# Optimization experiments

Measured on AMD Instinct MI355X. Metric: run time of the kernel, lower is better.

## Reference

```python
import math
import jax, jax.numpy as jnp
import numpy as np

PATCH_NUMS = (1, 2, 3, 4, 5, 6, 8, 10, 13, 16)
_lens = [p * p for p in PATCH_NUMS]
_cum = np.concatenate([[0], np.cumsum(_lens)])
BEGIN_ENDS = [(int(_cum[i]), int(_cum[i + 1])) for i in range(len(PATCH_NUMS))]
L_TOTAL = int(_cum[-1])  # 680

B, C = 32, 1024
S, P, M, R, NCAT = 10, 8, 4, 8, 22
SLOTS = P * M  # 32 slots per scale
MEM_RANK = 64
ALPHA_HID = 128


def setup_inputs() -> dict:
    key = jax.random.key(0)
    ks = jax.random.split(key, 24)
    inp = {}
    inp['x'] = jax.random.normal(ks[0], (B, L_TOTAL, C), jnp.float32)
    # -1 means CFG-unconditional sample (no category memory)
    inp['category_ids'] = jax.random.randint(ks[1], (B,), -1, NCAT)
    # shared memory, orthogonal-ish init rescaled to xavier std sqrt(2/(C+C))
    inp['shared_memory'] = jax.random.normal(ks[2], (S, SLOTS, C)) * math.sqrt(1.0 / C)
    inp['cat_A'] = jax.random.normal(ks[3], (NCAT, S, R)) * 0.01
    inp['cat_B'] = jax.random.normal(ks[4], (S, R, SLOTS * C)) * (1.0 / math.sqrt(R))
    inp['cat_emb'] = jax.random.normal(ks[5], (NCAT, C)) * 0.02
    inp['scale_emb'] = jax.random.normal(ks[6], (S, C)) * 0.02
    inp['Wq'] = jax.random.normal(ks[7], (C, C)) * (1.0 / math.sqrt(C))
    inp['Wk'] = jax.random.normal(ks[8], (C, C)) * (1.0 / math.sqrt(C))
    inp['Wv'] = jax.random.normal(ks[9], (C, C)) * (1.0 / math.sqrt(C))
    inp['aW1'] = jax.random.normal(ks[10], (3 * C, ALPHA_HID)) * (1.0 / math.sqrt(3 * C))
    inp['ab1'] = jnp.zeros((ALPHA_HID,), jnp.float32)
    inp['aW2'] = jax.random.normal(ks[11], (ALPHA_HID, 1)) * 0.01  # init zeros in torch; small random to exercise math
    inp['ab2'] = jnp.full((1,), -1.0, jnp.float32)
    inp['kW1'] = jax.random.normal(ks[12], (C, MEM_RANK)) * (1.0 / math.sqrt(C))
    inp['kb1'] = jnp.zeros((MEM_RANK,), jnp.float32)
    inp['kW2'] = jax.random.normal(ks[13], (MEM_RANK, C)) * (1.0 / math.sqrt(MEM_RANK))
    inp['kb2'] = jnp.zeros((C,), jnp.float32)
    inp['vW1'] = jax.random.normal(ks[14], (C, MEM_RANK)) * (1.0 / math.sqrt(C))
    inp['vb1'] = jnp.zeros((MEM_RANK,), jnp.float32)
    inp['vW2'] = jax.random.normal(ks[15], (MEM_RANK, C)) * (1.0 / math.sqrt(MEM_RANK))
    inp['vb2'] = jnp.zeros((C,), jnp.float32)
    inp['gk_logit'] = jnp.float32(-2.0)  # block_idx=0, depth=16
    inp['gv_logit'] = jnp.float32(-2.0)
    inp['log_temp'] = jnp.float32(math.log(0.1))
    return inp


def reference(x, category_ids, shared_memory, cat_A, cat_B, cat_emb, scale_emb,
              Wq, Wk, Wv, aW1, ab1, aW2, ab2,
              kW1, kb1, kW2, kb2, vW1, vb1, vW2, vb2,
              gk_logit, gv_logit, log_temp):
    Bb, L, Cc = x.shape
    temp = jnp.clip(jnp.exp(log_temp), 0.05, 1.0)
    inv_sqrt_c = 1.0 / math.sqrt(Cc)

    query = x @ Wq                              # [B, L, C]
    shared_k = shared_memory @ Wk               # [S, slots, C]
    shared_v = shared_memory @ Wv

    valid = (category_ids >= 0)                 # [B]
    cid = jnp.clip(category_ids, 0, None)
    a_all = cat_A[cid]                          # [B, S, R]
    ce = cat_emb[cid]                           # [B, C]

    outs = []
    for i, (s, e) in enumerate(BEGIN_ENDS):
        q = query[:, s:e, :]                    # [B, Ls, C]
        Ls = e - s
        V = i + 1                               # visible scales
        # --- shared retrieval over visible slots ---
        ks_ = shared_k[:V].reshape(V * SLOTS, Cc)
        vs_ = shared_v[:V].reshape(V * SLOTS, Cc)
        attn_s = jax.nn.softmax((q @ ks_.T) * inv_sqrt_c / temp, axis=-1)
        o_s = attn_s @ vs_                      # [B, Ls, C]
        # --- per-category memory: shared + low-rank residual ---
        delta = jnp.einsum('bvr,vrd->bvd', a_all[:, :V], cat_B[:V])
        delta = delta.reshape(Bb, V, SLOTS, Cc)
        cat_mem = (shared_memory[:V][None] + delta).reshape(Bb, V * SLOTS, Cc)
        kc = cat_mem @ Wk                       # [B, Vs, C]
        vc = cat_mem @ Wv
        attn_c = jax.nn.softmax(jnp.einsum('bld,bsd->bls', q, kc) * inv_sqrt_c / temp, axis=-1)
        o_c = jnp.einsum('bls,bsd->bld', attn_c, vc)
        # --- learned alpha blend (zeroed for invalid / CFG categories) ---
        ai = jnp.concatenate([
            q,
            jnp.broadcast_to(ce[:, None, :], (Bb, Ls, Cc)),
            jnp.broadcast_to(scale_emb[i][None, None, :], (Bb, Ls, Cc)),
        ], axis=-1)                             # [B, Ls, 3C]
        h = jax.nn.gelu(ai @ aW1 + ab1, approximate=False)
        alpha = jax.nn.sigmoid(h @ aW2 + ab2)   # [B, Ls, 1]
        alpha = jnp.where(valid[:, None, None], alpha, 0.0)
        outs.append(o_s + alpha * (o_c - o_s))

    mem = jnp.concatenate(outs, axis=1)         # [B, L, C]
    mem_k = jax.nn.sigmoid(gk_logit) * ((mem @ kW1 + kb1) @ kW2 + kb2)
    mem_v = jax.nn.sigmoid(gv_logit) * ((mem @ vW1 + vb1) @ vW2 + vb2)
    zero = jnp.float32(0.0)
    return mem_k, mem_v, zero, zero
```

## Files before the change

### kernel.cpp

```cpp
#include <hip/hip_runtime.h>
#include <math.h>

#define NB 32
#define NC 1024
#define LTOT 680

typedef unsigned short u16;
typedef __bf16 bf16x8 __attribute__((ext_vector_type(8)));
typedef float floatx4 __attribute__((ext_vector_type(4)));

__device__ __forceinline__ u16 f2bf(float f)
{
    union { float f; unsigned u; } v; v.f = f;
    unsigned u = v.u;
    u += 0x7FFFu + ((u >> 16) & 1u);
    return (u16)(u >> 16);
}

__device__ __forceinline__ float bf2f(unsigned u)
{
    union { unsigned u; float f; } v; v.u = u << 16; return v.f;
}

__device__ __forceinline__ void gload16(const u16* g, u16* l)
{
    typedef __attribute__((address_space(1))) const void gv_t;
    typedef __attribute__((address_space(3))) void lv_t;
    __builtin_amdgcn_global_load_lds(
        (gv_t*)(unsigned long long)(const void*)g,
        (lv_t*)(unsigned int)(unsigned long long)(void*)l,
        16, 0, 0);
}

__device__ __forceinline__ void slot_decode(int s, int* prow, int* pcq)
{
    *prow = ((s >> 7) << 4) | (s & 15);
    *pcq  = (((s >> 6) & 1) << 2) | ((s >> 4) & 3);
}

__device__ __forceinline__ void slot_decode256(int s, int* prow, int* pcq)
{
    *prow = ((s >> 6) << 4) | (s & 15);
    *pcq  = (s >> 4) & 3;
}

#define WAIT_VM8()  asm volatile("s_waitcnt vmcnt(8)" ::: "memory")
#define WAIT_VM4()  asm volatile("s_waitcnt vmcnt(4)" ::: "memory")
#define WAIT_VM0()  asm volatile("s_waitcnt vmcnt(0)" ::: "memory")
#define BAR()       __builtin_amdgcn_s_barrier()
#define SCHEDB()    __builtin_amdgcn_sched_barrier(0)

template<int OUTBF>
__global__ __launch_bounds__(512) void gemm256(
    const u16* __restrict__ A, const u16* __restrict__ BT,
    float* __restrict__ C, int M, int N, int K, int lda,
    const float* __restrict__ bias, const float* __restrict__ scale_logit)
{
    __shared__ __align__(16) u16 As[2][8192];
    __shared__ __align__(16) u16 Bs[2][8192];

    const int tid  = threadIdx.x;
    const int m0   = blockIdx.y << 8;
    const int n0   = blockIdx.x << 8;
    const int wave = tid >> 6;
    const int lane = tid & 63;
    const int mh   = wave & 1;
    const int nh   = wave >> 1;
    const int lbase = (wave << 6) * 8;

    const u16* aSrc[2];
    const u16* bSrc[2];
#pragma unroll
    for (int p = 0; p < 2; ++p) {
        int s = tid + (p << 9), row, cq;
        slot_decode256(s, &row, &cq);
        int gr = m0 + row; if (gr > M - 1) gr = M - 1;
        aSrc[p] = A + (size_t)gr * lda + (cq << 3);
        int gn = n0 + row; if (gn > N - 1) gn = N - 1;
        bSrc[p] = BT + (size_t)gn * K + (cq << 3);
    }

    floatx4 acc[8][4];
#pragma unroll
    for (int i = 0; i < 8; ++i)
#pragma unroll
        for (int j = 0; j < 4; ++j) acc[i][j] = (floatx4){0.f, 0.f, 0.f, 0.f};

#pragma unroll
    for (int p = 0; p < 2; ++p) gload16(aSrc[p], &As[0][lbase + (p << 12)]);
#pragma unroll
    for (int p = 0; p < 2; ++p) gload16(bSrc[p], &Bs[0][lbase + (p << 12)]);

    const int nt = K >> 5;
    for (int t = 0; t < nt; ++t) {
        const int cur = t & 1;
        if (t + 1 < nt) {
            const int kk = (t + 1) << 5;
#pragma unroll
            for (int p = 0; p < 2; ++p) gload16(aSrc[p] + kk, &As[cur ^ 1][lbase + (p << 12)]);
#pragma unroll
            for (int p = 0; p < 2; ++p) gload16(bSrc[p] + kk, &Bs[cur ^ 1][lbase + (p << 12)]);
            WAIT_VM4();
        } else {
            WAIT_VM0();
        }
        BAR(); SCHEDB();
        {
            bf16x8 a[8], b[4];
#pragma unroll
            for (int i = 0; i < 8; ++i)
                a[i] = *(const bf16x8*)&As[cur][((((mh << 3) + i) << 6) + lane) * 8];
#pragma unroll
            for (int j = 0; j < 4; ++j)
                b[j] = *(const bf16x8*)&Bs[cur][((((nh << 2) + j) << 6) + lane) * 8];
#pragma unroll
            for (int i = 0; i < 8; ++i)
#pragma unroll
                for (int j = 0; j < 4; ++j)
                    acc[i][j] = __builtin_amdgcn_mfma_f32_16x16x32_bf16(a[i], b[j], acc[i][j], 0, 0, 0);
        }
        SCHEDB(); BAR();
    }

    float scale = 1.f;
    if (scale_logit) scale = 1.f / (1.f + __expf(-scale_logit[0]));
    const int col = lane & 15, rquad = lane >> 4;
#pragma unroll
    for (int i = 0; i < 8; ++i) {
#pragma unroll
        for (int j = 0; j < 4; ++j) {
#pragma unroll
            for (int r = 0; r < 4; ++r) {
                int gr = m0 + (mh << 7) + (i << 4) + (rquad << 2) + r;
                int gc = n0 + (nh << 6) + (j << 4) + col;
                if (gr < M && gc < N) {
                    float bb = bias ? bias[gc] : 0.f;
                    float val = scale * (acc[i][j][r] + bb);
                    if (OUTBF) ((u16*)C)[(size_t)gr * N + gc] = f2bf(val);
                    else       C[(size_t)gr * N + gc] = val;
                }
            }
        }
    }
}

__global__ __launch_bounds__(512) void gemm256_logits(
    const u16* __restrict__ Q, const u16* __restrict__ skb,
    const u16* __restrict__ kcb, float* __restrict__ out)
{
    __shared__ __align__(16) u16 As[2][8192];
    __shared__ __align__(16) u16 Bs[2][8192];

    const int tid  = threadIdx.x;
    const int m0   = blockIdx.y << 8;
    const int n0   = blockIdx.x << 8;
    const int b    = blockIdx.z;
    const int wave = tid >> 6;
    const int lane = tid & 63;
    const int mh   = wave & 1;
    const int nh   = wave >> 1;
    const int lbase = (wave << 6) * 8;

    const u16* Ab = Q   + (size_t)b * 680 * 1024;
    const u16* KC = kcb + (size_t)b * 320 * 1024;

    const u16* aSrc[2];
    const u16* bSrc[2];
#pragma unroll
    for (int p = 0; p < 2; ++p) {
        int s = tid + (p << 9), row, cq;
        slot_decode256(s, &row, &cq);
        int gr = m0 + row; if (gr > 679) gr = 679;
        aSrc[p] = Ab + (size_t)gr * 1024 + (cq << 3);
        int gn = n0 + row; if (gn > 639) gn = 639;
        bSrc[p] = ((gn < 320) ? (skb + (size_t)gn * 1024)
                              : (KC + (size_t)(gn - 320) * 1024)) + (cq << 3);
    }

    floatx4 acc[8][4];
#pragma unroll
    for (int i = 0; i < 8; ++i)
#pragma unroll
        for (int j = 0; j < 4; ++j) acc[i][j] = (floatx4){0.f, 0.f, 0.f, 0.f};

#pragma unroll
    for (int p = 0; p < 2; ++p) gload16(aSrc[p], &As[0][lbase + (p << 12)]);
#pragma unroll
    for (int p = 0; p < 2; ++p) gload16(bSrc[p], &Bs[0][lbase + (p << 12)]);

    for (int t = 0; t < 32; ++t) {
        const int cur = t & 1;
        if (t < 31) {
            const int kk = (t + 1) << 5;
#pragma unroll
            for (int p = 0; p < 2; ++p) gload16(aSrc[p] + kk, &As[cur ^ 1][lbase + (p << 12)]);
#pragma unroll
            for (int p = 0; p < 2; ++p) gload16(bSrc[p] + kk, &Bs[cur ^ 1][lbase + (p << 12)]);
            WAIT_VM4();
        } else {
            WAIT_VM0();
        }
        BAR(); SCHEDB();
        {
            bf16x8 a[8], bb[4];
#pragma unroll
            for (int i = 0; i < 8; ++i)
                a[i] = *(const bf16x8*)&As[cur][((((mh << 3) + i) << 6) + lane) * 8];
#pragma unroll
            for (int j = 0; j < 4; ++j)
                bb[j] = *(const bf16x8*)&Bs[cur][((((nh << 2) + j) << 6) + lane) * 8];
#pragma unroll
            for (int i = 0; i < 8; ++i)
#pragma unroll
                for (int j = 0; j < 4; ++j)
                    acc[i][j] = __builtin_amdgcn_mfma_f32_16x16x32_bf16(a[i], bb[j], acc[i][j], 0, 0, 0);
        }
        SCHEDB(); BAR();
    }

    const int col = lane & 15, rquad = lane >> 4;
#pragma unroll
    for (int i = 0; i < 8; ++i)
#pragma unroll
        for (int j = 0; j < 4; ++j)
#pragma unroll
            for (int r = 0; r < 4; ++r) {
                int gr = m0 + (mh << 7) + (i << 4) + (rquad << 2) + r;
                int gc = n0 + (nh << 6) + (j << 4) + col;
                if (gr < 680 && gc < 640)
                    out[((size_t)b * 680 + gr) * 640 + gc] = acc[i][j][r];
            }
}

__global__ __launch_bounds__(512) void gemm256_pv(
    const u16* __restrict__ P, const u16* __restrict__ svT,
    const u16* __restrict__ vcT, u16* __restrict__ out)
{
    __shared__ __align__(16) u16 As[2][8192];
    __shared__ __align__(16) u16 Bs[2][8192];

    const int tid  = threadIdx.x;
    const int m0   = blockIdx.y << 8;
    const int n0   = blockIdx.x << 8;
    const int b    = blockIdx.z;
    const int wave = tid >> 6;
    const int lane = tid & 63;
    const int mh   = wave & 1;
    const int nh   = wave >> 1;
    const int lbase = (wave << 6) * 8;

    const u16* aSrc[2];
    const u16* bSrcS[2];
    const u16* bSrcC[2];
#pragma unroll
    for (int p = 0; p < 2; ++p) {
        int s = tid + (p << 9), row, cq;
        slot_decode256(s, &row, &cq);
        int gr = m0 + row; if (gr > 679) gr = 679;
        aSrc[p] = P + ((size_t)b * 680 + gr) * 1280 + (cq << 3);
        int gn = n0 + row;
        bSrcS[p] = svT + (size_t)gn * 320 + (cq << 3);
        bSrcC[p] = vcT + ((size_t)b * 1024 + gn) * 320 + (cq << 3);
    }

    floatx4 acc[8][4];
#pragma unroll
    for (int i = 0; i < 8; ++i)
#pragma unroll
        for (int j = 0; j < 4; ++j) acc[i][j] = (floatx4){0.f, 0.f, 0.f, 0.f};

#pragma unroll
    for (int p = 0; p < 2; ++p) gload16(aSrc[p], &As[0][lbase + (p << 12)]);
#pragma unroll
    for (int p = 0; p < 2; ++p) gload16(bSrcS[p], &Bs[0][lbase + (p << 12)]);

    for (int t = 0; t < 20; ++t) {
        const int cur = t & 1;
        if (t < 19) {
            const int tn = t + 1;
            const int kk = tn << 5;
#pragma unroll
            for (int p = 0; p < 2; ++p) gload16(aSrc[p] + kk, &As[cur ^ 1][lbase + (p << 12)]);
#pragma unroll
            for (int p = 0; p < 2; ++p) {
                const u16* bp = (tn < 10) ? (bSrcS[p] + kk) : (bSrcC[p] + ((tn - 10) << 5));
                gload16(bp, &Bs[cur ^ 1][lbase + (p << 12)]);
            }
            WAIT_VM4();
        } else {
            WAIT_VM0();
        }
        BAR(); SCHEDB();
        {
            bf16x8 a[8], bb[4];
#pragma unroll
            for (int i = 0; i < 8; ++i)
                a[i] = *(const bf16x8*)&As[cur][((((mh << 3) + i) << 6) + lane) * 8];
#pragma unroll
            for (int j = 0; j < 4; ++j)
                bb[j] = *(const bf16x8*)&Bs[cur][((((nh << 2) + j) << 6) + lane) * 8];
#pragma unroll
            for (int i = 0; i < 8; ++i)
#pragma unroll
                for (int j = 0; j < 4; ++j)
                    acc[i][j] = __builtin_amdgcn_mfma_f32_16x16x32_bf16(a[i], bb[j], acc[i][j], 0, 0, 0);
        }
        SCHEDB(); BAR();
    }

    const int col = lane & 15, rquad = lane >> 4;
#pragma unroll
    for (int i = 0; i < 8; ++i)
#pragma unroll
        for (int j = 0; j < 4; ++j)
#pragma unroll
            for (int r = 0; r < 4; ++r) {
                int gr = m0 + (mh << 7) + (i << 4) + (rquad << 2) + r;
                int gc = n0 + (nh << 6) + (j << 4) + col;
                if (gr < 680)
                    out[((size_t)b * 680 + gr) * 1024 + gc] = f2bf(acc[i][j][r]);
            }
}

template<int OUTBF>
__global__ __launch_bounds__(256) void gemm_mfma(
    const u16* __restrict__ A, const u16* __restrict__ BT,
    float* __restrict__ C, int M, int N, int K, int lda,
    const float* __restrict__ bias, const float* __restrict__ scale_logit)
{
    __shared__ __align__(16) u16 As[2][8192];
    __shared__ __align__(16) u16 Bs[2][8192];

    const int tid  = threadIdx.x;
    const int m0   = blockIdx.y << 7;
    const int n0   = blockIdx.x << 7;
    const int wave = tid >> 6;
    const int lane = tid & 63;
    const int mh   = wave & 1;
    const int nh   = wave >> 1;
    const int lbase = (wave << 6) * 8;

    const u16* aSrc[4];
    const u16* bSrc[4];
#pragma unroll
    for (int p = 0; p < 4; ++p) {
        int s = tid + (p << 8), row, cq;
        slot_decode(s, &row, &cq);
        int gr = m0 + row; if (gr > M - 1) gr = M - 1;
        aSrc[p] = A + (size_t)gr * lda + (cq << 3);
        int gn = n0 + row; if (gn > N - 1) gn = N - 1;
        bSrc[p] = BT + (size_t)gn * K + (cq << 3);
    }

    floatx4 acc[4][4];
#pragma unroll
    for (int i = 0; i < 4; ++i)
#pragma unroll
        for (int j = 0; j < 4; ++j) acc[i][j] = (floatx4){0.f, 0.f, 0.f, 0.f};

#pragma unroll
    for (int p = 0; p < 4; ++p) gload16(aSrc[p], &As[0][lbase + (p << 11)]);
#pragma unroll
    for (int p = 0; p < 4; ++p) gload16(bSrc[p], &Bs[0][lbase + (p << 11)]);

    const int nt = K >> 6;
    for (int t = 0; t < nt; ++t) {
        const int cur = t & 1;
        if (t + 1 < nt) {
            const int kk = (t + 1) << 6;
#pragma unroll
            for (int p = 0; p < 4; ++p) gload16(aSrc[p] + kk, &As[cur ^ 1][lbase + (p << 11)]);
#pragma unroll
            for (int p = 0; p < 4; ++p) gload16(bSrc[p] + kk, &Bs[cur ^ 1][lbase + (p << 11)]);
            WAIT_VM8();
        } else {
            WAIT_VM0();
        }
        BAR(); SCHEDB();
#pragma unroll
        for (int kh = 0; kh < 2; ++kh) {
            bf16x8 a[4], b[4];
#pragma unroll
            for (int i = 0; i < 4; ++i)
                a[i] = *(const bf16x8*)&As[cur][(((((mh << 2) + i) << 1) | kh) * 64 + lane) * 8];
#pragma unroll
            for (int j = 0; j < 4; ++j)
                b[j] = *(const bf16x8*)&Bs[cur][(((((nh << 2) + j) << 1) | kh) * 64 + lane) * 8];
#pragma unroll
            for (int i = 0; i < 4; ++i)
#pragma unroll
                for (int j = 0; j < 4; ++j)
                    acc[i][j] = __builtin_amdgcn_mfma_f32_16x16x32_bf16(a[i], b[j], acc[i][j], 0, 0, 0);
        }
        SCHEDB(); BAR();
    }

    float scale = 1.f;
    if (scale_logit) scale = 1.f / (1.f + __expf(-scale_logit[0]));
    const int col = lane & 15, rquad = lane >> 4;
#pragma unroll
    for (int i = 0; i < 4; ++i) {
#pragma unroll
        for (int j = 0; j < 4; ++j) {
#pragma unroll
            for (int r = 0; r < 4; ++r) {
                int gr = m0 + (mh << 6) + (i << 4) + (rquad << 2) + r;
                int gc = n0 + (nh << 6) + (j << 4) + col;
                if (gr < M && gc < N) {
                    float bb = bias ? bias[gc] : 0.f;
                    float val = scale * (acc[i][j][r] + bb);
                    if (OUTBF) ((u16*)C)[(size_t)gr * N + gc] = f2bf(val);
                    else       C[(size_t)gr * N + gc] = val;
                }
            }
        }
    }
}

__global__ __launch_bounds__(256) void gemm_halpha(
    const u16* __restrict__ Q, const u16* __restrict__ W,
    const float* __restrict__ ceW, const float* __restrict__ seW,
    const int* __restrict__ cat_ids, u16* __restrict__ h)
{
    __shared__ __align__(16) u16 As[2][8192];
    __shared__ __align__(16) u16 Bs[2][8192];

    const int tid  = threadIdx.x;
    const int m0   = blockIdx.x << 7;
    const int wave = tid >> 6;
    const int lane = tid & 63;
    const int mh   = wave & 1;
    const int nh   = wave >> 1;
    const int lbase = (wave << 6) * 8;

    const u16* aSrc[4];
    const u16* bSrc[4];
#pragma unroll
    for (int p = 0; p < 4; ++p) {
        int s = tid + (p << 8), row, cq;
        slot_decode(s, &row, &cq);
        aSrc[p] = Q + (size_t)(m0 + row) * 1024 + (cq << 3);
        bSrc[p] = W + (size_t)row * 1024 + (cq << 3);
    }

    floatx4 acc[4][4];
#pragma unroll
    for (int i = 0; i < 4; ++i)
#pragma unroll
        for (int j = 0; j < 4; ++j) acc[i][j] = (floatx4){0.f, 0.f, 0.f, 0.f};

#pragma unroll
    for (int p = 0; p < 4; ++p) gload16(aSrc[p], &As[0][lbase + (p << 11)]);
#pragma unroll
    for (int p = 0; p < 4; ++p) gload16(bSrc[p], &Bs[0][lbase + (p << 11)]);

    for (int t = 0; t < 16; ++t) {
        const int cur = t & 1;
        if (t < 15) {
            const int kk = (t + 1) << 6;
#pragma unroll
            for (int p = 0; p < 4; ++p) gload16(aSrc[p] + kk, &As[cur ^ 1][lbase + (p << 11)]);
#pragma unroll
            for (int p = 0; p < 4; ++p) gload16(bSrc[p] + kk, &Bs[cur ^ 1][lbase + (p << 11)]);
            WAIT_VM8();
        } else {
            WAIT_VM0();
        }
        BAR(); SCHEDB();
#pragma unroll
        for (int kh = 0; kh < 2; ++kh) {
            bf16x8 a[4], bb[4];
#pragma unroll
            for (int i = 0; i < 4; ++i)
                a[i] = *(const bf16x8*)&As[cur][(((((mh << 2) + i) << 1) | kh) * 64 + lane) * 8];
#pragma unroll
            for (int j = 0; j < 4; ++j)
                bb[j] = *(const bf16x8*)&Bs[cur][(((((nh << 2) + j) << 1) | kh) * 64 + lane) * 8];
#pragma unroll
            for (int i = 0; i < 4; ++i)
#pragma unroll
                for (int j = 0; j < 4; ++j)
                    acc[i][j] = __builtin_amdgcn_mfma_f32_16x16x32_bf16(a[i], bb[j], acc[i][j], 0, 0, 0);
        }
        SCHEDB(); BAR();
    }

    const int se_[9] = {1,5,14,30,55,91,155,255,424};
    const int col = lane & 15, rquad = lane >> 4;
#pragma unroll
    for (int i = 0; i < 4; ++i) {
#pragma unroll
        for (int r = 0; r < 4; ++r) {
            int gr = m0 + (mh << 6) + (i << 4) + (rquad << 2) + r;
            int b  = gr / 680;
            int l  = gr - b * 680;
            int isc = 0;
#pragma unroll
            for (int k = 0; k < 9; ++k) if (l >= se_[k]) isc = k + 1;
            int cid = cat_ids[b]; if (cid < 0) cid = 0;
            const float* cw = ceW + cid * 128;
            const float* sw = seW + isc * 128;
#pragma unroll
            for (int j = 0; j < 4; ++j) {
                int gc = (nh << 6) + (j << 4) + col;
                float val = acc[i][j][r] + cw[gc] + sw[gc];
                float g = 0.5f * val * (1.0f + erff(val * 0.70710678118654752f));
                h[(size_t)gr * 128 + gc] = f2bf(g);
            }
        }
    }
}

__global__ __launch_bounds__(256) void alpha_reduce(
    const u16* __restrict__ h, const float* __restrict__ aW2,
    const float* __restrict__ ab2, const int* __restrict__ cat_ids,
    float* __restrict__ alpha)
{
    const int wave = threadIdx.x >> 6;
    const int lane = threadIdx.x & 63;
    const int row  = (blockIdx.x << 2) + wave;

    const unsigned pk = *(const unsigned*)(h + (size_t)row * 128 + (lane << 1));
    float s = bf2f(pk) * aW2[lane << 1] + bf2f(pk >> 16) * aW2[(lane << 1) + 1];
#pragma unroll
    for (int k = 32; k >= 1; k >>= 1) s += __shfl_xor(s, k);
    if (lane == 0) {
        int b = row / 680;
        float al = 0.f;
        if (cat_ids[b] >= 0) al = 1.f / (1.f + expf(-(s + ab2[0])));
        alpha[row] = al;
    }
}

__global__ __launch_bounds__(256) void softmax_kernel(
    float* __restrict__ logits, const float* __restrict__ alpha,
    const float* __restrict__ log_temp)
{
    const int tid  = threadIdx.x;
    const int w    = tid >> 6;
    const int lane = tid & 63;
    const int b    = blockIdx.y;
    const int l    = (blockIdx.x << 2) + w;

    const int se[10] = {1,5,14,30,55,91,155,255,424,680};
    int isc = 0;
#pragma unroll
    for (int k = 0; k < 9; ++k) if (l >= se[k]) isc = k + 1;
    const int NK = (isc + 1) << 5;

    float temp = __expf(log_temp[0]);
    temp = fminf(fmaxf(temp, 0.05f), 1.0f);
    const float Ksc = 0.03125f / temp;

    float* row = logits + ((size_t)b * 680 + l) * 640;

    float ls[5], lc[5];
#pragma unroll
    for (int u = 0; u < 5; ++u) {
        int j = lane + (u << 6);
        bool v = j < NK;
        ls[u] = v ? row[j]       : -1e30f;
        lc[u] = v ? row[320 + j] : -1e30f;
    }
    float mxs = -1e30f, mxc = -1e30f;
#pragma unroll
    for (int u = 0; u < 5; ++u) { mxs = fmaxf(mxs, ls[u]); mxc = fmaxf(mxc, lc[u]); }
#pragma unroll
    for (int k = 32; k >= 1; k >>= 1) {
        mxs = fmaxf(mxs, __shfl_xor(mxs, k));
        mxc = fmaxf(mxc, __shfl_xor(mxc, k));
    }
    float es[5], ec[5], ss = 0.f, sc = 0.f;
#pragma unroll
    for (int u = 0; u < 5; ++u) {
        int j = lane + (u << 6);
        bool v = j < NK;
        es[u] = v ? __expf((ls[u] - mxs) * Ksc) : 0.f;
        ec[u] = v ? __expf((lc[u] - mxc) * Ksc) : 0.f;
        ss += es[u]; sc += ec[u];
    }
#pragma unroll
    for (int k = 32; k >= 1; k >>= 1) {
        ss += __shfl_xor(ss, k);
        sc += __shfl_xor(sc, k);
    }
    const float al = alpha[b * LTOT + l];
    const float wS = (1.f - al) / ss;
    const float wC = al / sc;

    u16* po = (u16*)row;
#pragma unroll
    for (int u = 0; u < 5; ++u) {
        int j = lane + (u << 6);
        po[j]       = f2bf(es[u] * wS);
        po[320 + j] = f2bf(ec[u] * wC);
    }
}

__global__ __launch_bounds__(256) void castbf(
    const float* __restrict__ in, u16* __restrict__ out, int n4)
{
    int i = blockIdx.x * 256 + threadIdx.x;
    const int stride = gridDim.x * 256;
    for (; i < n4; i += stride) {
        const float4 v = ((const float4*)in)[i];
        uint2 o;
        o.x = (unsigned)f2bf(v.x) | ((unsigned)f2bf(v.y) << 16);
        o.y = (unsigned)f2bf(v.z) | ((unsigned)f2bf(v.w) << 16);
        ((uint2*)out)[i] = o;
    }
}

__global__ __launch_bounds__(256) void tcast(
    const float* __restrict__ in, u16* __restrict__ out, int R, int Cc)
{
    __shared__ float t[32][33];
    const int bx = blockIdx.x * 32;
    const int by = blockIdx.y * 32;
    const int x = threadIdx.x & 31;
    const int y0 = threadIdx.x >> 5;
#pragma unroll
    for (int yy = y0; yy < 32; yy += 8)
        t[yy][x] = (by + yy < R && bx + x < Cc)
                 ? in[(size_t)(by + yy) * Cc + bx + x] : 0.f;
    __syncthreads();
#pragma unroll
    for (int yy = y0; yy < 32; yy += 8)
        if (bx + yy < Cc && by + x < R)
            out[(size_t)(bx + yy) * R + by + x] = f2bf(t[x][yy]);
}

__global__ __launch_bounds__(256) void transpose32(
    const float* __restrict__ in, float* __restrict__ out, int R, int Cc)
{
    __shared__ float t[32][33];
    const int bx = blockIdx.x * 32;
    const int by = blockIdx.y * 32;
    const int x = threadIdx.x & 31;
    const int y0 = threadIdx.x >> 5;
#pragma unroll
    for (int yy = y0; yy < 32; yy += 8)
        t[yy][x] = (by + yy < R && bx + x < Cc)
                 ? in[(size_t)(by + yy) * Cc + bx + x] : 0.f;
    __syncthreads();
#pragma unroll
    for (int yy = y0; yy < 32; yy += 8)
        if (bx + yy < Cc && by + x < R)
            out[(size_t)(bx + yy) * R + by + x] = t[x][yy];
}

__global__ __launch_bounds__(256) void build_kc2(
    const float* __restrict__ sk, const float* __restrict__ catBK,
    const float* __restrict__ cat_A, const int* __restrict__ cat_ids,
    u16* __restrict__ kc)
{
    __shared__ float bk[8][1024];
    __shared__ float skr[1024];
    __shared__ float aS[32][8];
    const int jrow = blockIdx.x;
    const int v = jrow >> 5, slot = jrow & 31;
    const int tid = threadIdx.x;

    for (int idx = tid; idx < 2048; idx += 256) {
        int r = idx >> 8, c4 = (idx & 255) << 2;
        *(float4*)&bk[r][c4] =
            *(const float4*)(catBK + (size_t)((v * 8 + r) * 32 + slot) * 1024 + c4);
    }
    *(float4*)&skr[tid << 2] = *(const float4*)(sk + (size_t)jrow * 1024 + (tid << 2));
    {
        int b = tid >> 3, r = tid & 7;
        int cid = cat_ids[b]; if (cid < 0) cid = 0;
        aS[b][r] = cat_A[(cid * 10 + v) * 8 + r];
    }
    __syncthreads();

    const int c = tid << 2;
    const float4 base = *(const float4*)&skr[c];
    for (int b = 0; b < 32; ++b) {
        float4 acc = base;
#pragma unroll
        for (int r = 0; r < 8; ++r) {
            const float a = aS[b][r];
            const float4 bv = *(const float4*)&bk[r][c];
            acc.x = fmaf(a, bv.x, acc.x);
            acc.y = fmaf(a, bv.y, acc.y);
            acc.z = fmaf(a, bv.z, acc.z);
            acc.w = fmaf(a, bv.w, acc.w);
        }
        uint2 pk;
        pk.x = (unsigned)f2bf(acc.x) | ((unsigned)f2bf(acc.y) << 16);
        pk.y = (unsigned)f2bf(acc.z) | ((unsigned)f2bf(acc.w) << 16);
        *(uint2*)(kc + ((size_t)b * 320 + jrow) * 1024 + c) = pk;
    }
}

__global__ __launch_bounds__(320) void build_vcT2(
    const float* __restrict__ svT, const float* __restrict__ catBVT,
    const float* __restrict__ cat_A, const int* __restrict__ cat_ids,
    u16* __restrict__ vcT)
{
    __shared__ float rowS[2560];
    __shared__ float svr[320];
    __shared__ float aS[32][80];
    const int c = blockIdx.x;
    const int tid = threadIdx.x;

    for (int idx = tid; idx < 2560; idx += 320)
        rowS[idx] = catBVT[(size_t)c * 2560 + idx];
    svr[tid] = svT[(size_t)c * 320 + tid];
    for (int idx = tid; idx < 2560; idx += 320) {
        int b = idx / 80, t = idx - b * 80;
        int cid = cat_ids[b]; if (cid < 0) cid = 0;
        aS[b][t] = cat_A[cid * 80 + t];
    }
    __syncthreads();

    const int j = tid, v = j >> 5, slot = j & 31;
    const float base = svr[j];
    const float* rp = &rowS[v * 256 + slot];
    for (int b = 0; b < 32; ++b) {
        float acc = base;
        const float* ap = &aS[b][v * 8];
#pragma unroll
        for (int r = 0; r < 8; ++r)
            acc = fmaf(ap[r], rp[r * 32], acc);
        vcT[((size_t)b * 1024 + c) * 320 + j] = f2bf(acc);
    }
}

__global__ void concat_bias(const float* __restrict__ a,
                            const float* __restrict__ b, float* __restrict__ o)
{
    int t = threadIdx.x;
    if (t < 64) o[t] = a[t];
    else if (t < 128) o[t] = b[t - 64];
}

__global__ void tail_zero(float* p)
{
    if (threadIdx.x < 2) p[threadIdx.x] = 0.f;
}

extern "C" void kernel_launch(void* const* d_in, const int* in_sizes, int n_in,
                              void* d_out, int out_size, void* d_ws, size_t ws_size,
                              hipStream_t stream)
{
    (void)in_sizes; (void)n_in;
    const float* x         = (const float*)d_in[0];
    const int*   cat_ids   = (const int*)  d_in[1];
    const float* sm        = (const float*)d_in[2];
    const float* cat_A     = (const float*)d_in[3];
    const float* cat_B     = (const float*)d_in[4];
    const float* cat_emb   = (const float*)d_in[5];
    const float* scale_emb = (const float*)d_in[6];
    const float* Wq        = (const float*)d_in[7];
    const float* Wk        = (const float*)d_in[8];
    const float* Wv        = (const float*)d_in[9];
    const float* aW1       = (const float*)d_in[10];
    const float* ab1       = (const float*)d_in[11];
    const float* aW2       = (const float*)d_in[12];
    const float* ab2       = (const float*)d_in[13];
    const float* kW1       = (const float*)d_in[14];
    const float* kb1       = (const float*)d_in[15];
    const float* kW2       = (const float*)d_in[16];
    const float* kb2       = (const float*)d_in[17];
    const float* vW1       = (const float*)d_in[18];
    const float* vb1       = (const float*)d_in[19];
    const float* vW2       = (const float*)d_in[20];
    const float* vb2       = (const float*)d_in[21];
    const float* gk        = (const float*)d_in[22];
    const float* gv        = (const float*)d_in[23];
    const float* log_temp  = (const float*)d_in[24];

    float* out   = (float*)d_out;
    float* memb  = out;
    float* outv  = out + (size_t)21760 * 1024;

    float* w      = (float*)d_ws;
    u16*   kc_bf  = (u16*)w;
    u16*   vcT_bf = (u16*)(w + 5242880);
    float* sk     = w + 10485760;
    float* sv     = w + 10813440;
    float* svT    = w + 11141120;
    u16*   sk_bf  = (u16*)(w + 11468800);
    u16*   svT_bf = (u16*)(w + 11632640);
    float* alph   = w + 11796480;
    float* logits = w + 11859200;
    float* tail0  = w + 25785600;
    u16*   aW1topT = (u16*)tail0;
    u16*   aW1midT = (u16*)(tail0 + 65536);
    u16*   aW1botT = (u16*)(tail0 + 131072);
    float* ceW    = tail0 + 196608;
    float* seW    = tail0 + 199424;
    float* cb     = tail0 + 200704;
    u16*   h_bf   = (u16*)(tail0 + 200832);
    u16*   catB_bf = (u16*)(w + 27379072);
    u16*   sm_bf  = (u16*)(w + 28689792);
    u16*   ce_bf  = (u16*)(w + 28853632);
    u16*   se_bf  = (u16*)(w + 28864896);
    if (ws_size < (size_t)29881600 * 4) return;
    if (out_size < 2 * 21760 * 1024 + 2) return;

    u16*   x_bf   = (u16*)logits;
    float* bufA   = logits + 5570560;
    float* bufB   = bufA + 2621440;
    float* catBVT = bufB + 2621440;
    u16*   WqT    = (u16*)w;
    u16*   WkT    = WqT + 1048576;
    u16*   WvT    = WkT + 1048576;
    u16*   kW1T   = (u16*)sv;
    u16*   vW1T   = kW1T + 65536;
    u16*   kW2T   = vW1T + 65536;
    u16*   vW2T   = kW2T + 65536;
    u16*   bufAB_bf = (u16*)w;
    u16*   mem_bf = (u16*)memb;
    u16*   query_bf = (u16*)outv;

    const dim3 blk256(256);
    const dim3 blk512(512);

    castbf<<<dim3(2048), blk256, 0, stream>>>(x, x_bf, 21760 * 1024 / 4);
    castbf<<<dim3(320), blk256, 0, stream>>>(sm, sm_bf, 320 * 1024 / 4);
    castbf<<<dim3(2048), blk256, 0, stream>>>(cat_B, catB_bf, 2560 * 1024 / 4);
    castbf<<<dim3(22), blk256, 0, stream>>>(cat_emb, ce_bf, 22 * 1024 / 4);
    castbf<<<dim3(10), blk256, 0, stream>>>(scale_emb, se_bf, 10 * 1024 / 4);
    tcast<<<dim3(32, 32), blk256, 0, stream>>>(Wq, WqT, 1024, 1024);
    tcast<<<dim3(32, 32), blk256, 0, stream>>>(Wk, WkT, 1024, 1024);
    tcast<<<dim3(32, 32), blk256, 0, stream>>>(Wv, WvT, 1024, 1024);
    tcast<<<dim3(4, 32), blk256, 0, stream>>>(aW1,              aW1topT, 1024, 128);
    tcast<<<dim3(4, 32), blk256, 0, stream>>>(aW1 + 1024 * 128, aW1midT, 1024, 128);
    tcast<<<dim3(4, 32), blk256, 0, stream>>>(aW1 + 2048 * 128, aW1botT, 1024, 128);

    gemm256<1><<<dim3(4, 85), blk512, 0, stream>>>(x_bf,    WqT, (float*)query_bf, 21760, 1024, 1024, 1024, nullptr, nullptr);
    gemm256<0><<<dim3(4, 2),  blk512, 0, stream>>>(sm_bf,   WkT, sk,   320,  1024, 1024, 1024, nullptr, nullptr);
    gemm256<0><<<dim3(4, 2),  blk512, 0, stream>>>(sm_bf,   WvT, sv,   320,  1024, 1024, 1024, nullptr, nullptr);
    gemm256<0><<<dim3(4, 10), blk512, 0, stream>>>(catB_bf, WkT, bufA, 2560, 1024, 1024, 1024, nullptr, nullptr);
    gemm256<0><<<dim3(4, 10), blk512, 0, stream>>>(catB_bf, WvT, bufB, 2560, 1024, 1024, 1024, nullptr, nullptr);

    gemm_mfma<0><<<dim3(1, 1), blk256, 0, stream>>>(ce_bf, aW1midT, ceW, 22, 128, 1024, 1024, nullptr, nullptr);
    gemm_mfma<0><<<dim3(1, 1), blk256, 0, stream>>>(se_bf, aW1botT, seW, 10, 128, 1024, 1024, ab1, nullptr);

    castbf<<<dim3(320), blk256, 0, stream>>>(sk, sk_bf, 320 * 1024 / 4);
    transpose32<<<dim3(32, 10), blk256, 0, stream>>>(sv, svT, 320, 1024);
    tcast<<<dim3(32, 10), blk256, 0, stream>>>(sv, svT_bf, 320, 1024);
    transpose32<<<dim3(32, 80), blk256, 0, stream>>>(bufB, catBVT, 2560, 1024);
    tcast<<<dim3(2, 32), blk256, 0, stream>>>(kW1, kW1T, 1024, 64);
    tcast<<<dim3(2, 32), blk256, 0, stream>>>(vW1, vW1T, 1024, 64);
    tcast<<<dim3(32, 2), blk256, 0, stream>>>(kW2, kW2T, 64, 1024);
    tcast<<<dim3(32, 2), blk256, 0, stream>>>(vW2, vW2T, 64, 1024);
    concat_bias<<<dim3(1), dim3(128), 0, stream>>>(kb1, vb1, cb);

    build_kc2<<<dim3(320), blk256, 0, stream>>>(sk, bufA, cat_A, cat_ids, kc_bf);
    build_vcT2<<<dim3(1024), dim3(320), 0, stream>>>(svT, catBVT, cat_A, cat_ids, vcT_bf);

    gemm_halpha<<<dim3(170), blk256, 0, stream>>>(query_bf, aW1topT, ceW, seW, cat_ids, h_bf);
    alpha_reduce<<<dim3(5440), blk256, 0, stream>>>(h_bf, aW2, ab2, cat_ids, alph);

    gemm256_logits<<<dim3(3, 3, NB), blk512, 0, stream>>>(query_bf, sk_bf, kc_bf, logits);
    softmax_kernel<<<dim3(170, NB), blk256, 0, stream>>>(logits, alph, log_temp);
    gemm256_pv<<<dim3(4, 3, NB), blk512, 0, stream>>>((const u16*)logits, svT_bf, vcT_bf, mem_bf);

    gemm_mfma<1><<<dim3(1, 170), blk256, 0, stream>>>(mem_bf, kW1T, (float*)bufAB_bf, 21760, 128, 1024, 1024, cb, nullptr);
    gemm256<0><<<dim3(4, 85), blk512, 0, stream>>>(bufAB_bf,      kW2T, memb, 21760, 1024, 64, 128, kb2, gk);
    gemm256<0><<<dim3(4, 85), blk512, 0, stream>>>(bufAB_bf + 64, vW2T, outv, 21760, 1024, 64, 128, vb2, gv);

    tail_zero<<<1, 64, 0, stream>>>(out + (size_t)2 * 21760 * 1024);
}
```

Before: 993.3 us.

## Deepen GEMM global-to-LDS pipelines to four stages and retile small GEMMs

Every MFMA GEMM kernel now uses a 4-slot LDS ring with three K-tiles prefetched ahead, and the vmcnt wait depth is chosen from the number of tiles still in flight. This replaces double buffering and aims to hide more global-load latency. The 128-tile GEMM switches to a K-step of 32 with half the loads per stage, and the mid-sized weight GEMMs (sk, sv, catB) move from 256-tiles to 128-tiles to launch more blocks. LDS per block doubles to 128KB in the 256-tile kernels, which limits occupancy to one block per CU.

```diff
diff --git a/kernel.cpp b/kernel.cpp
--- a/kernel.cpp
+++ b/kernel.cpp
@@ -32,32 +32,30 @@
         16, 0, 0);
 }
 
-__device__ __forceinline__ void slot_decode(int s, int* prow, int* pcq)
-{
-    *prow = ((s >> 7) << 4) | (s & 15);
-    *pcq  = (((s >> 6) & 1) << 2) | ((s >> 4) & 3);
-}
-
 __device__ __forceinline__ void slot_decode256(int s, int* prow, int* pcq)
 {
     *prow = ((s >> 6) << 4) | (s & 15);
     *pcq  = (s >> 4) & 3;
 }
 
-#define WAIT_VM8()  asm volatile("s_waitcnt vmcnt(8)" ::: "memory")
-#define WAIT_VM4()  asm volatile("s_waitcnt vmcnt(4)" ::: "memory")
-#define WAIT_VM0()  asm volatile("s_waitcnt vmcnt(0)" ::: "memory")
+__device__ __forceinline__ void wait_tiles(int fl)
+{
+    if (fl >= 3)      asm volatile("s_waitcnt vmcnt(12)" ::: "memory");
+    else if (fl == 2) asm volatile("s_waitcnt vmcnt(8)"  ::: "memory");
+    else if (fl == 1) asm volatile("s_waitcnt vmcnt(4)"  ::: "memory");
+    else              asm volatile("s_waitcnt vmcnt(0)"  ::: "memory");
+}
 #define BAR()       __builtin_amdgcn_s_barrier()
 #define SCHEDB()    __builtin_amdgcn_sched_barrier(0)
 
 template<int OUTBF>
-__global__ __launch_bounds__(512) void gemm256(
+__global__ __launch_bounds__(512) void gemm256d(
     const u16* __restrict__ A, const u16* __restrict__ BT,
     float* __restrict__ C, int M, int N, int K, int lda,
     const float* __restrict__ bias, const float* __restrict__ scale_logit)
 {
-    __shared__ __align__(16) u16 As[2][8192];
-    __shared__ __align__(16) u16 Bs[2][8192];
+    __shared__ __align__(16) u16 As[4][8192];
+    __shared__ __align__(16) u16 Bs[4][8192];
 
     const int tid  = threadIdx.x;
     const int m0   = blockIdx.y << 8;
@@ -86,25 +84,25 @@
 #pragma unroll
         for (int j = 0; j < 4; ++j) acc[i][j] = (floatx4){0.f, 0.f, 0.f, 0.f};
 
-#pragma unroll
-    for (int p = 0; p < 2; ++p) gload16(aSrc[p], &As[0][lbase + (p << 12)]);
-#pragma unroll
-    for (int p = 0; p < 2; ++p) gload16(bSrc[p], &Bs[0][lbase + (p << 12)]);
+    auto STAGE = [&](int tn) {
+        const int kk = tn << 5;
+        u16* da = &As[tn & 3][lbase];
+        u16* db = &Bs[tn & 3][lbase];
+#pragma unroll
+        for (int p = 0; p < 2; ++p) gload16(aSrc[p] + kk, da + (p << 12));
+#pragma unroll
+        for (int p = 0; p < 2; ++p) gload16(bSrc[p] + kk, db + (p << 12));
+    };
 
     const int nt = K >> 5;
+    for (int pre = 0; pre < 3 && pre < nt; ++pre) STAGE(pre);
+
     for (int t = 0; t < nt; ++t) {
-        const int cur = t & 1;
-        if (t + 1 < nt) {
-            const int kk = (t + 1) << 5;
-#pragma unroll
-            for (int p = 0; p < 2; ++p) gload16(aSrc[p] + kk, &As[cur ^ 1][lbase + (p << 12)]);
-#pragma unroll
-            for (int p = 0; p < 2; ++p) gload16(bSrc[p] + kk, &Bs[cur ^ 1][lbase + (p << 12)]);
-            WAIT_VM4();
-        } else {
-            WAIT_VM0();
-        }
+        if (t + 3 < nt) STAGE(t + 3);
+        int fl = nt - 1 - t; if (fl > 3) fl = 3;
+        wait_tiles(fl);
         BAR(); SCHEDB();
+        const int cur = t & 3;
         {
             bf16x8 a[8], b[4];
 #pragma unroll
@@ -144,12 +142,12 @@
     }
 }
 
-__global__ __launch_bounds__(512) void gemm256_logits(
+__global__ __launch_bounds__(512) void gemm_logits(
     const u16* __restrict__ Q, const u16* __restrict__ skb,
     const u16* __restrict__ kcb, float* __restrict__ out)
 {
-    __shared__ __align__(16) u16 As[2][8192];
-    __shared__ __align__(16) u16 Bs[2][8192];
+    __shared__ __align__(16) u16 As[4][8192];
+    __shared__ __align__(16) u16 Bs[4][8192];
 
     const int tid  = threadIdx.x;
     const int m0   = blockIdx.y << 8;
@@ -183,24 +181,24 @@
 #pragma unroll
         for (int j = 0; j < 4; ++j) acc[i][j] = (floatx4){0.f, 0.f, 0.f, 0.f};
 
-#pragma unroll
-    for (int p = 0; p < 2; ++p) gload16(aSrc[p], &As[0][lbase + (p << 12)]);
-#pragma unroll
-    for (int p = 0; p < 2; ++p) gload16(bSrc[p], &Bs[0][lbase + (p << 12)]);
+    auto STAGE = [&](int tn) {
+        const int kk = tn << 5;
+        u16* da = &As[tn & 3][lbase];
+        u16* db = &Bs[tn & 3][lbase];
+#pragma unroll
+        for (int p = 0; p < 2; ++p) gload16(aSrc[p] + kk, da + (p << 12));
+#pragma unroll
+        for (int p = 0; p < 2; ++p) gload16(bSrc[p] + kk, db + (p << 12));
+    };
+
+    for (int pre = 0; pre < 3; ++pre) STAGE(pre);
 
     for (int t = 0; t < 32; ++t) {
-        const int cur = t & 1;
-        if (t < 31) {
-            const int kk = (t + 1) << 5;
-#pragma unroll
-            for (int p = 0; p < 2; ++p) gload16(aSrc[p] + kk, &As[cur ^ 1][lbase + (p << 12)]);
-#pragma unroll
-            for (int p = 0; p < 2; ++p) gload16(bSrc[p] + kk, &Bs[cur ^ 1][lbase + (p << 12)]);
-            WAIT_VM4();
-        } else {
-            WAIT_VM0();
-        }
+        if (t + 3 < 32) STAGE(t + 3);
+        int fl = 31 - t; if (fl > 3) fl = 3;
+        wait_tiles(fl);
         BAR(); SCHEDB();
+        const int cur = t & 3;
         {
             bf16x8 a[8], bb[4];
 #pragma unroll
@@ -232,12 +230,12 @@
             }
 }
 
-__global__ __launch_bounds__(512) void gemm256_pv(
+__global__ __launch_bounds__(512) void gemm_pv(
     const u16* __restrict__ P, const u16* __restrict__ svT,
     const u16* __restrict__ vcT, u16* __restrict__ out)
 {
-    __shared__ __align__(16) u16 As[2][8192];
-    __shared__ __align__(16) u16 Bs[2][8192];
+    __shared__ __align__(16) u16 As[4][8192];
+    __shared__ __align__(16) u16 Bs[4][8192];
 
     const int tid  = threadIdx.x;
     const int m0   = blockIdx.y << 8;
@@ -269,28 +267,27 @@
 #pragma unroll
         for (int j = 0; j < 4; ++j) acc[i][j] = (floatx4){0.f, 0.f, 0.f, 0.f};
 
-#pragma unroll
-    for (int p = 0; p < 2; ++p) gload16(aSrc[p], &As[0][lbase + (p << 12)]);
-#pragma unroll
-    for (int p = 0; p < 2; ++p) gload16(bSrcS[p], &Bs[0][lbase + (p << 12)]);
+    auto STAGE = [&](int tn) {
+        const int kk = tn << 5;
+        u16* da = &As[tn & 3][lbase];
+        u16* db = &Bs[tn & 3][lbase];
+#pragma unroll
+        for (int p = 0; p < 2; ++p) gload16(aSrc[p] + kk, da + (p << 12));
+#pragma unroll
+        for (int p = 0; p < 2; ++p) {
+            const u16* bp = (tn < 10) ? (bSrcS[p] + kk) : (bSrcC[p] + (kk - 320));
+            gload16(bp, db + (p << 12));
+        }
+    };
+
+    for (int pre = 0; pre < 3; ++pre) STAGE(pre);
 
     for (int t = 0; t < 20; ++t) {
-        const int cur = t & 1;
-        if (t < 19) {
-            const int tn = t + 1;
-            const int kk = tn << 5;
-#pragma unroll
-            for (int p = 0; p < 2; ++p) gload16(aSrc[p] + kk, &As[cur ^ 1][lbase + (p << 12)]);
-#pragma unroll
-            for (int p = 0; p < 2; ++p) {
-                const u16* bp = (tn < 10) ? (bSrcS[p] + kk) : (bSrcC[p] + ((tn - 10) << 5));
-                gload16(bp, &Bs[cur ^ 1][lbase + (p << 12)]);
-            }
-            WAIT_VM4();
-        } else {
-            WAIT_VM0();
-        }
+        if (t + 3 < 20) STAGE(t + 3);
+        int fl = 19 - t; if (fl > 3) fl = 3;
+        wait_tiles(fl);
         BAR(); SCHEDB();
+        const int cur = t & 3;
         {
             bf16x8 a[8], bb[4];
 #pragma unroll
@@ -323,13 +320,13 @@
 }
 
 template<int OUTBF>
-__global__ __launch_bounds__(256) void gemm_mfma(
+__global__ __launch_bounds__(256) void gemm128d(
     const u16* __restrict__ A, const u16* __restrict__ BT,
     float* __restrict__ C, int M, int N, int K, int lda,
     const float* __restrict__ bias, const float* __restrict__ scale_logit)
 {
-    __shared__ __align__(16) u16 As[2][8192];
-    __shared__ __align__(16) u16 Bs[2][8192];
+    __shared__ __align__(16) u16 As[4][4096];
+    __shared__ __align__(16) u16 Bs[4][4096];
 
     const int tid  = threadIdx.x;
     const int m0   = blockIdx.y << 7;
@@ -340,12 +337,12 @@
     const int nh   = wave >> 1;
     const int lbase = (wave << 6) * 8;
 
-    const u16* aSrc[4];
-    const u16* bSrc[4];
-#pragma unroll
-    for (int p = 0; p < 4; ++p) {
+    const u16* aSrc[2];
+    const u16* bSrc[2];
+#pragma unroll
+    for (int p = 0; p < 2; ++p) {
         int s = tid + (p << 8), row, cq;
-        slot_decode(s, &row, &cq);
+        slot_decode256(s, &row, &cq);
         int gr = m0 + row; if (gr > M - 1) gr = M - 1;
         aSrc[p] = A + (size_t)gr * lda + (cq << 3);
         int gn = n0 + row; if (gn > N - 1) gn = N - 1;
@@ -358,34 +355,33 @@
 #pragma unroll
         for (int j = 0; j < 4; ++j) acc[i][j] = (floatx4){0.f, 0.f, 0.f, 0.f};
 
-#pragma unroll
-    for (int p = 0; p < 4; ++p) gload16(aSrc[p], &As[0][lbase + (p << 11)]);
-#pragma unroll
-    for (int p = 0; p < 4; ++p) gload16(bSrc[p], &Bs[0][lbase + (p << 11)]);
-
-    const int nt = K >> 6;
+    auto STAGE = [&](int tn) {
+        const int kk = tn << 5;
+        u16* da = &As[tn & 3][lbase];
+        u16* db = &Bs[tn & 3][lbase];
+#pragma unroll
+        for (int p = 0; p < 2; ++p) gload16(aSrc[p] + kk, da + (p << 11));
+#pragma unroll
+        for (int p = 0; p < 2; ++p) gload16(bSrc[p] + kk, db + (p << 11));
+    };
+
+    const int nt = K >> 5;
+    for (int pre = 0; pre < 3 && pre < nt; ++pre) STAGE(pre);
+
     for (int t = 0; t < nt; ++t) {
-        const int cur = t & 1;
-        if (t + 1 < nt) {
-            const int kk = (t + 1) << 6;
-#pragma unroll
-            for (int p = 0; p < 4; ++p) gload16(aSrc[p] + kk, &As[cur ^ 1][lbase + (p << 11)]);
-#pragma unroll
-            for (int p = 0; p < 4; ++p) gload16(bSrc[p] + kk, &Bs[cur ^ 1][lbase + (p << 11)]);
-            WAIT_VM8();
-        } else {
-            WAIT_VM0();
-        }
+        if (t + 3 < nt) STAGE(t + 3);
+        int fl = nt - 1 - t; if (fl > 3) fl = 3;
+        wait_tiles(fl);
         BAR(); SCHEDB();
-#pragma unroll
-        for (int kh = 0; kh < 2; ++kh) {
+        const int cur = t & 3;
+        {
             bf16x8 a[4], b[4];
 #pragma unroll
             for (int i = 0; i < 4; ++i)
-                a[i] = *(const bf16x8*)&As[cur][(((((mh << 2) + i) << 1) | kh) * 64 + lane) * 8];
+                a[i] = *(const bf16x8*)&As[cur][((((mh << 2) + i) << 6) + lane) * 8];
 #pragma unroll
             for (int j = 0; j < 4; ++j)
-                b[j] = *(const bf16x8*)&Bs[cur][(((((nh << 2) + j) << 1) | kh) * 64 + lane) * 8];
+                b[j] = *(const bf16x8*)&Bs[cur][((((nh << 2) + j) << 6) + lane) * 8];
 #pragma unroll
             for (int i = 0; i < 4; ++i)
 #pragma unroll
@@ -422,8 +418,8 @@
     const float* __restrict__ ceW, const float* __restrict__ seW,
     const int* __restrict__ cat_ids, u16* __restrict__ h)
 {
-    __shared__ __align__(16) u16 As[2][8192];
-    __shared__ __align__(16) u16 Bs[2][8192];
+    __shared__ __align__(16) u16 As[4][4096];
+    __shared__ __align__(16) u16 Bs[4][4096];
 
     const int tid  = threadIdx.x;
     const int m0   = blockIdx.x << 7;
@@ -433,12 +429,12 @@
     const int nh   = wave >> 1;
     const int lbase = (wave << 6) * 8;
 
-    const u16* aSrc[4];
-    const u16* bSrc[4];
-#pragma unroll
-    for (int p = 0; p < 4; ++p) {
+    const u16* aSrc[2];
+    const u16* bSrc[2];
+#pragma unroll
+    for (int p = 0; p < 2; ++p) {
         int s = tid + (p << 8), row, cq;
-        slot_decode(s, &row, &cq);
+        slot_decode256(s, &row, &cq);
         aSrc[p] = Q + (size_t)(m0 + row) * 1024 + (cq << 3);
         bSrc[p] = W + (size_t)row * 1024 + (cq << 3);
     }
@@ -449,33 +445,32 @@
 #pragma unroll
         for (int j = 0; j < 4; ++j) acc[i][j] = (floatx4){0.f, 0.f, 0.f, 0.f};
 
-#pragma unroll
-    for (int p = 0; p < 4; ++p) gload16(aSrc[p], &As[0][lbase + (p << 11)]);
-#pragma unroll
-    for (int p = 0; p < 4; ++p) gload16(bSrc[p], &Bs[0][lbase + (p << 11)]);
-
-    for (int t = 0; t < 16; ++t) {
-        const int cur = t & 1;
-        if (t < 15) {
-            const int kk = (t + 1) << 6;
-#pragma unroll
-            for (int p = 0; p < 4; ++p) gload16(aSrc[p] + kk, &As[cur ^ 1][lbase + (p << 11)]);
-#pragma unroll
-            for (int p = 0; p < 4; ++p) gload16(bSrc[p] + kk, &Bs[cur ^ 1][lbase + (p << 11)]);
-            WAIT_VM8();
-        } else {
-            WAIT_VM0();
-        }
+    auto STAGE = [&](int tn) {
+        const int kk = tn << 5;
+        u16* da = &As[tn & 3][lbase];
+        u16* db = &Bs[tn & 3][lbase];
+#pragma unroll
+        for (int p = 0; p < 2; ++p) gload16(aSrc[p] + kk, da + (p << 11));
+#pragma unroll
+        for (int p = 0; p < 2; ++p) gload16(bSrc[p] + kk, db + (p << 11));
+    };
+
+    for (int pre = 0; pre < 3; ++pre) STAGE(pre);
+
+    for (int t = 0; t < 32; ++t) {
+        if (t + 3 < 32) STAGE(t + 3);
+        int fl = 31 - t; if (fl > 3) fl = 3;
+        wait_tiles(fl);
         BAR(); SCHEDB();
-#pragma unroll
-        for (int kh = 0; kh < 2; ++kh) {
+        const int cur = t & 3;
+        {
             bf16x8 a[4], bb[4];
 #pragma unroll
             for (int i = 0; i < 4; ++i)
-                a[i] = *(const bf16x8*)&As[cur][(((((mh << 2) + i) << 1) | kh) * 64 + lane) * 8];
+                a[i] = *(const bf16x8*)&As[cur][((((mh << 2) + i) << 6) + lane) * 8];
 #pragma unroll
             for (int j = 0; j < 4; ++j)
-                bb[j] = *(const bf16x8*)&Bs[cur][(((((nh << 2) + j) << 1) | kh) * 64 + lane) * 8];
+                bb[j] = *(const bf16x8*)&Bs[cur][((((nh << 2) + j) << 6) + lane) * 8];
 #pragma unroll
             for (int i = 0; i < 4; ++i)
 #pragma unroll
@@ -831,14 +826,14 @@
     tcast<<<dim3(4, 32), blk256, 0, stream>>>(aW1 + 1024 * 128, aW1midT, 1024, 128);
     tcast<<<dim3(4, 32), blk256, 0, stream>>>(aW1 + 2048 * 128, aW1botT, 1024, 128);
 
-    gemm256<1><<<dim3(4, 85), blk512, 0, stream>>>(x_bf,    WqT, (float*)query_bf, 21760, 1024, 1024, 1024, nullptr, nullptr);
-    gemm256<0><<<dim3(4, 2),  blk512, 0, stream>>>(sm_bf,   WkT, sk,   320,  1024, 1024, 1024, nullptr, nullptr);
-    gemm256<0><<<dim3(4, 2),  blk512, 0, stream>>>(sm_bf,   WvT, sv,   320,  1024, 1024, 1024, nullptr, nullptr);
-    gemm256<0><<<dim3(4, 10), blk512, 0, stream>>>(catB_bf, WkT, bufA, 2560, 1024, 1024, 1024, nullptr, nullptr);
-    gemm256<0><<<dim3(4, 10), blk512, 0, stream>>>(catB_bf, WvT, bufB, 2560, 1024, 1024, 1024, nullptr, nullptr);
-
-    gemm_mfma<0><<<dim3(1, 1), blk256, 0, stream>>>(ce_bf, aW1midT, ceW, 22, 128, 1024, 1024, nullptr, nullptr);
-    gemm_mfma<0><<<dim3(1, 1), blk256, 0, stream>>>(se_bf, aW1botT, seW, 10, 128, 1024, 1024, ab1, nullptr);
+    gemm256d<1><<<dim3(4, 85), blk512, 0, stream>>>(x_bf,    WqT, (float*)query_bf, 21760, 1024, 1024, 1024, nullptr, nullptr);
+    gemm128d<0><<<dim3(8, 3),  blk256, 0, stream>>>(sm_bf,   WkT, sk,   320,  1024, 1024, 1024, nullptr, nullptr);
+    gemm128d<0><<<dim3(8, 3),  blk256, 0, stream>>>(sm_bf,   WvT, sv,   320,  1024, 1024, 1024, nullptr, nullptr);
+    gemm128d<0><<<dim3(8, 20), blk256, 0, stream>>>(catB_bf, WkT, bufA, 2560, 1024, 1024, 1024, nullptr, nullptr);
+    gemm128d<0><<<dim3(8, 20), blk256, 0, stream>>>(catB_bf, WvT, bufB, 2560, 1024, 1024, 1024, nullptr, nullptr);
+
+    gemm128d<0><<<dim3(1, 1), blk256, 0, stream>>>(ce_bf, aW1midT, ceW, 22, 128, 1024, 1024, nullptr, nullptr);
+    gemm128d<0><<<dim3(1, 1), blk256, 0, stream>>>(se_bf, aW1botT, seW, 10, 128, 1024, 1024, ab1, nullptr);
 
     castbf<<<dim3(320), blk256, 0, stream>>>(sk, sk_bf, 320 * 1024 / 4);
     transpose32<<<dim3(32, 10), blk256, 0, stream>>>(sv, svT, 320, 1024);
@@ -856,13 +851,13 @@
     gemm_halpha<<<dim3(170), blk256, 0, stream>>>(query_bf, aW1topT, ceW, seW, cat_ids, h_bf);
     alpha_reduce<<<dim3(5440), blk256, 0, stream>>>(h_bf, aW2, ab2, cat_ids, alph);
 
-    gemm256_logits<<<dim3(3, 3, NB), blk512, 0, stream>>>(query_bf, sk_bf, kc_bf, logits);
+    gemm_logits<<<dim3(3, 3, NB), blk512, 0, stream>>>(query_bf, sk_bf, kc_bf, logits);
     softmax_kernel<<<dim3(170, NB), blk256, 0, stream>>>(logits, alph, log_temp);
-    gemm256_pv<<<dim3(4, 3, NB), blk512, 0, stream>>>((const u16*)logits, svT_bf, vcT_bf, mem_bf);
-
-    gemm_mfma<1><<<dim3(1, 170), blk256, 0, stream>>>(mem_bf, kW1T, (float*)bufAB_bf, 21760, 128, 1024, 1024, cb, nullptr);
-    gemm256<0><<<dim3(4, 85), blk512, 0, stream>>>(bufAB_bf,      kW2T, memb, 21760, 1024, 64, 128, kb2, gk);
-    gemm256<0><<<dim3(4, 85), blk512, 0, stream>>>(bufAB_bf + 64, vW2T, outv, 21760, 1024, 64, 128, vb2, gv);
+    gemm_pv<<<dim3(4, 3, NB), blk512, 0, stream>>>((const u16*)logits, svT_bf, vcT_bf, mem_bf);
+
+    gemm128d<1><<<dim3(1, 170), blk256, 0, stream>>>(mem_bf, kW1T, (float*)bufAB_bf, 21760, 128, 1024, 1024, cb, nullptr);
+    gemm256d<0><<<dim3(4, 85), blk512, 0, stream>>>(bufAB_bf,      kW2T, memb, 21760, 1024, 64, 128, kb2, gk);
+    gemm256d<0><<<dim3(4, 85), blk512, 0, stream>>>(bufAB_bf + 64, vW2T, outv, 21760, 1024, 64, 128, vb2, gv);
 
     tail_zero<<<1, 64, 0, stream>>>(out + (size_t)2 * 21760 * 1024);
 }
```

After: 897.6 us. 9.6% less time.
